# Kernel optimization log

Hardware: AMD Instinct MI355X
Metric: run time of the kernel (lower is better)

Reference implementation:

```python
import jax, jax.numpy as jnp
import numpy as np

NEG_SLOPE = 0.2


def setup_inputs() -> dict:
    key = jax.random.key(0)
    ks = jax.random.split(key, 9)
    N, E, D, H, C, G = 50000, 800000, 128, 4, 32, 64
    x = jax.random.normal(ks[0], (N, D), dtype=jnp.float32)
    edge_index = jax.random.randint(ks[1], (2, E), 0, N, dtype=jnp.int64)
    batch_ids = jnp.sort(jax.random.randint(ks[2], (N,), 0, G, dtype=jnp.int64))
    Wl = jax.random.normal(ks[3], (D, H * C), dtype=jnp.float32) / np.sqrt(D)
    Wr = jax.random.normal(ks[4], (D, H * C), dtype=jnp.float32) / np.sqrt(D)
    att = jax.random.normal(ks[5], (H, C), dtype=jnp.float32) / np.sqrt(C)
    bias_conv = jax.random.normal(ks[6], (H * C,), dtype=jnp.float32) * 0.01
    W_mlp = jax.random.normal(ks[7], (H * C, H * C), dtype=jnp.float32) / np.sqrt(H * C)
    b_mlp = jax.random.normal(ks[8], (H * C,), dtype=jnp.float32) * 0.01
    return {"x": x, "edge_index": edge_index, "batch_ids": batch_ids,
            "num_graphs": G, "Wl": Wl, "Wr": Wr, "att": att,
            "bias_conv": bias_conv, "W_mlp": W_mlp, "b_mlp": b_mlp}


def gatv2_forward(x, edge_index, batch_ids, num_graphs, Wl, Wr, att, bias_conv, W_mlp, b_mlp):
    N = x.shape[0]
    H, C = att.shape
    # add self loops (PyG default)
    loops = jnp.arange(N, dtype=edge_index.dtype)
    src = jnp.concatenate([edge_index[0], loops])
    dst = jnp.concatenate([edge_index[1], loops])
    xl = (x @ Wl).reshape(N, H, C)  # source transform
    xr = (x @ Wr).reshape(N, H, C)  # target transform
    # GATv2 attention logits per edge/head
    e = jax.nn.leaky_relu(xl[src] + xr[dst], NEG_SLOPE)  # [E,H,C]
    logits = jnp.einsum('ehc,hc->eh', e, att)            # [E,H]
    # segment softmax over incoming edges of each dst node
    m = jax.ops.segment_max(logits, dst, num_segments=N)
    ex = jnp.exp(logits - m[dst])
    denom = jax.ops.segment_sum(ex, dst, num_segments=N)
    alpha = ex / denom[dst]                              # [E,H]
    # weighted scatter-sum of source features
    out = jax.ops.segment_sum(alpha[:, :, None] * xl[src], dst, num_segments=N)
    out = out.reshape(N, H * C) + bias_conv
    out = jax.nn.relu(out)
    # global max pool per graph
    pooled = jax.ops.segment_max(out, batch_ids, num_segments=num_graphs)
    return jax.nn.relu(pooled @ W_mlp + b_mlp)


def reference(x, edge_index, batch_ids, num_graphs, Wl, Wr, att, bias_conv, W_mlp, b_mlp):
    return gatv2_forward(x, edge_index, batch_ids, num_graphs, Wl, Wr, att,
                         bias_conv, W_mlp, b_mlp)
```

## Files before the change

kernel.cpp:

```cpp
#include <hip/hip_runtime.h>
#include <hip/hip_bf16.h>

#define NN 50000
#define EE 800000
#define HC 128
#define GG 64

#define NBLK 256
#define CHUNK (EE / NBLK)
#define NBUCK ((NN + 63) >> 6)
#define NTOT (NBUCK * NBLK)
#define NSB ((NTOT + 1023) / 1024)
#define ECAP 2048

typedef __attribute__((ext_vector_type(8))) short bf16x8;
typedef __attribute__((ext_vector_type(4))) float f32x4;
typedef _Float16 hv2 __attribute__((ext_vector_type(2)));

__device__ __forceinline__ float dpp4_redrow(float t) {
  t += __int_as_float(__builtin_amdgcn_update_dpp(0, __float_as_int(t), 0x111, 0xf, 0xf, true));
  t += __int_as_float(__builtin_amdgcn_update_dpp(0, __float_as_int(t), 0x112, 0xf, 0xf, true));
  t += __int_as_float(__builtin_amdgcn_update_dpp(0, __float_as_int(t), 0x114, 0xf, 0xf, true));
  t += __int_as_float(__builtin_amdgcn_update_dpp(0, __float_as_int(t), 0x118, 0xf, 0xf, true));
  return t;
}
__device__ __forceinline__ float bcast15(float t) {
  return __int_as_float(__builtin_amdgcn_ds_swizzle(__float_as_int(t), 0x1F0));
}

__device__ __forceinline__ unsigned pkbf(float lo, float hi) {
  __hip_bfloat162 h = __float22bfloat162_rn(float2{lo, hi});
  return *reinterpret_cast<unsigned*>(&h);
}
__device__ __forceinline__ unsigned pkhf(float lo, float hi) {
  hv2 h; h.x = (_Float16)lo; h.y = (_Float16)hi;
  return __builtin_bit_cast(unsigned, h);
}

__global__ __launch_bounds__(128) void prep_w(const float* __restrict__ Wl,
                                              const float* __restrict__ Wr,
                                              short* __restrict__ Wtb) {
  int c = blockIdx.x;
  int k = threadIdx.x;
  const float* W = (c < 128) ? Wl : Wr;
  float v = W[k * 128 + (c & 127)];
  Wtb[c * 128 + k] = (short)(pkbf(v, 0.f) & 0xFFFF);
}

__global__ __launch_bounds__(256) void gemm_xw(
    const float* __restrict__ x, const short* __restrict__ Wtb,
    _Float16* __restrict__ xlh, _Float16* __restrict__ xrh,
    const int* __restrict__ ei, int* __restrict__ H2T)
{
  __shared__ short xs[128 * 136];
  __shared__ int h[NBUCK];
  const int t = threadIdx.x;
  const int rowbase = blockIdx.x * 128;
#pragma unroll
  for (int i = 0; i < 16; ++i) {
    int fi = i * 256 + t;
    int row = fi >> 5, k4 = fi & 31;
    int ar = rowbase + row; if (ar >= NN) ar = NN - 1;
    float4 v = *(const float4*)(x + (size_t)ar * 128 + k4 * 4);
    uint2 p = { pkbf(v.x, v.y), pkbf(v.z, v.w) };
    *(uint2*)&xs[row * 136 + k4 * 4] = p;
  }
  __syncthreads();
  const int w = t >> 6, l = t & 63;
  const int lo16 = l & 15, hi = l >> 4;
  f32x4 accL[2][8], accR[2][8];
#pragma unroll
  for (int rf = 0; rf < 2; ++rf)
#pragma unroll
    for (int cf = 0; cf < 8; ++cf) {
      accL[rf][cf] = f32x4{0.f, 0.f, 0.f, 0.f};
      accR[rf][cf] = f32x4{0.f, 0.f, 0.f, 0.f};
    }

  const short* asrc0 = &xs[(w * 32 + lo16) * 136 + hi * 8];
  const short* asrc1 = asrc0 + 16 * 136;
#pragma unroll
  for (int ks = 0; ks < 4; ++ks) {
    bf16x8 a0 = *(const bf16x8*)(asrc0 + ks * 32);
    bf16x8 a1 = *(const bf16x8*)(asrc1 + ks * 32);
#pragma unroll
    for (int cf = 0; cf < 8; ++cf) {
      const short* bp = &Wtb[(cf * 16 + lo16) * 128 + ks * 32 + hi * 8];
      bf16x8 bL = *(const bf16x8*)bp;
      bf16x8 bR = *(const bf16x8*)(bp + 128 * 128);
      accL[0][cf] = __builtin_amdgcn_mfma_f32_16x16x32_bf16(a0, bL, accL[0][cf], 0, 0, 0);
      accL[1][cf] = __builtin_amdgcn_mfma_f32_16x16x32_bf16(a1, bL, accL[1][cf], 0, 0, 0);
      accR[0][cf] = __builtin_amdgcn_mfma_f32_16x16x32_bf16(a0, bR, accR[0][cf], 0, 0, 0);
      accR[1][cf] = __builtin_amdgcn_mfma_f32_16x16x32_bf16(a1, bR, accR[1][cf], 0, 0, 0);
    }
  }
#pragma unroll
  for (int rf = 0; rf < 2; ++rf)
#pragma unroll
    for (int cf = 0; cf < 8; ++cf)
#pragma unroll
      for (int r = 0; r < 4; ++r) {
        int row = rowbase + w * 32 + rf * 16 + hi * 4 + r;
        if (row < NN) {
          int col = cf * 16 + lo16;
          xlh[(size_t)row * 128 + col] = (_Float16)accL[rf][cf][r];
          xrh[(size_t)row * 128 + col] = (_Float16)accR[rf][cf][r];
        }
      }
  int blk = blockIdx.x;
  if (blk < NBLK) {
    for (int b = t; b < NBUCK; b += 256) h[b] = 0;
    __syncthreads();
    int e0 = blk * CHUNK;
    for (int i = t; i < CHUNK; i += 256) {
      int d = ei[EE + e0 + i];
      atomicAdd(&h[d >> 6], 1);
    }
    __syncthreads();
    for (int b = t; b < NBUCK; b += 256) H2T[b * NBLK + blk] = h[b];
  }
}

__global__ __launch_bounds__(256) void scanA(const int* __restrict__ H2T,
                                             int* __restrict__ PS, int* __restrict__ bsum) {
  __shared__ int tmp[256];
  int t = threadIdx.x;
  int base = blockIdx.x * 1024 + t * 4;
  int4 v = {0, 0, 0, 0};
  if (base < NTOT) v = *(const int4*)&H2T[base];
  int local = v.x + v.y + v.z + v.w;
  tmp[t] = local; __syncthreads();
  for (int off = 1; off < 256; off <<= 1) {
    int xv = (t >= off) ? tmp[t - off] : 0; __syncthreads();
    tmp[t] += xv; __syncthreads();
  }
  int excl = tmp[t] - local;
  if (base < NTOT) {
    int4 o;
    o.x = excl; excl += v.x;
    o.y = excl; excl += v.y;
    o.z = excl; excl += v.z;
    o.w = excl;
    *(int4*)&PS[base] = o;
  }
  if (t == 255) bsum[blockIdx.x] = tmp[255];
}

__global__ __launch_bounds__(256) void scatter_coarse(const int* __restrict__ ei,
                                                      const int* __restrict__ PS,
                                                      const int* __restrict__ bsum,
                                                      int* __restrict__ ec) {
  __shared__ int colbase[NBUCK];
  __shared__ int cur[NBUCK];
  __shared__ int sb[NSB];
  __shared__ int stmp[256];
  int t = threadIdx.x, blk = blockIdx.x;
  int v = (t < NSB) ? bsum[t] : 0;
  stmp[t] = v; __syncthreads();
  for (int off = 1; off < 256; off <<= 1) {
    int xv = (t >= off) ? stmp[t - off] : 0; __syncthreads();
    stmp[t] += xv; __syncthreads();
  }
  if (t < NSB) sb[t] = stmp[t] - v;
  __syncthreads();
  for (int b = t; b < NBUCK; b += 256) {
    int L = b * NBLK + blk;
    colbase[b] = PS[L] + sb[L >> 10];
    cur[b] = 0;
  }
  __syncthreads();
  int e0 = blk * CHUNK;
  for (int i = t; i < CHUNK; i += 256) {
    int d = ei[EE + e0 + i], s = ei[e0 + i];
    int b = d >> 6;
    int r = atomicAdd(&cur[b], 1);
    ec[colbase[b] + r] = s | ((d & 63) << 16);
  }
}

__global__ __launch_bounds__(256) void fine_sort(const int* __restrict__ PS,
                                                 const int* __restrict__ bsum,
                                                 const int* __restrict__ ec,
                                                 int* __restrict__ rs, int* __restrict__ csr) {
  __shared__ int lbuf[ECAP];
  __shared__ int outb[ECAP + 64];
  __shared__ int fh[64], sexcl[65], cur2[64];
  __shared__ int sb[NSB];
  __shared__ int stmp[256];
  int t = threadIdx.x, b = blockIdx.x;
  int v = (t < NSB) ? bsum[t] : 0;
  stmp[t] = v; __syncthreads();
  for (int off = 1; off < 256; off <<= 1) {
    int xv = (t >= off) ? stmp[t - off] : 0; __syncthreads();
    stmp[t] += xv; __syncthreads();
  }
  if (t < NSB) sb[t] = stmp[t] - v;
  __syncthreads();
  int L0 = b * NBLK;
  int start = PS[L0] + sb[L0 >> 10];
  int end = (b + 1 < NBUCK) ? PS[L0 + NBLK] + sb[(L0 + NBLK) >> 10] : EE;
  int node0 = b << 6;
  int nl = NN - node0; if (nl > 64) nl = 64;
  int cnt = end - start; if (cnt > ECAP) cnt = ECAP;
  if (t < 64) { fh[t] = 0; cur2[t] = 0; }
  __syncthreads();
  for (int i = t; i < cnt; i += 256) {
    int p = ec[start + i];
    lbuf[i] = p;
    atomicAdd(&fh[(p >> 16) & 63], 1);
  }
  __syncthreads();
  if (t < 64) {
    int val = fh[t] + (t < nl ? 1 : 0);
    int w = val;
    for (int off = 1; off < 64; off <<= 1) {
      int u = __shfl_up(w, off);
      if (t >= off) w += u;
    }
    sexcl[t] = w - val;
    if (t == 63) sexcl[64] = w;
  }
  __syncthreads();
  int base = start + node0;
  if (t <= nl) rs[node0 + t] = base + sexcl[t];
  if (t < nl) {
    int r = atomicAdd(&cur2[t], 1);
    outb[sexcl[t] + r] = node0 + t;
  }
  for (int i = t; i < cnt; i += 256) {
    int p = lbuf[i];
    int f = (p >> 16) & 63;
    int r = atomicAdd(&cur2[f], 1);
    outb[sexcl[f] + r] = p & 0xFFFF;
  }
  __syncthreads();
  int tot = cnt + nl;
  for (int i = t; i < tot; i += 256) csr[base + i] = outb[i];
}

template<int M>
__device__ __forceinline__ void procM(const unsigned* wv, hv2 att2, hv2 xr2,
                                      float& s, float& a0, float& a1) {
  float tb[M];
#pragma unroll
  for (int i = 0; i < M; ++i) {
    hv2 v = __builtin_bit_cast(hv2, wv[i]);
    hv2 y = v + xr2;
    hv2 lr = __builtin_elementwise_max(y, y * (_Float16)0.2f);
    float td = __builtin_amdgcn_fdot2(lr, att2, 0.f, false);
    tb[i] = bcast15(dpp4_redrow(td));
  }
  float p[M];
#pragma unroll
  for (int i = 0; i < M; ++i) p[i] = __builtin_amdgcn_exp2f(tb[i]);
#pragma unroll
  for (int i = 0; i < M; ++i) {
    hv2 v = __builtin_bit_cast(hv2, wv[i]);
    s += p[i];
    a0 = fmaf(p[i], (float)v.x, a0);
    a1 = fmaf(p[i], (float)v.y, a1);
  }
}

__global__ __launch_bounds__(256) void gat_agg(
    const unsigned* __restrict__ xlu, const unsigned* __restrict__ xru,
    const int* __restrict__ rs, const int* __restrict__ csr,
    const float* __restrict__ att, const float* __restrict__ bias,
    unsigned* __restrict__ outh)
{
  int wid = threadIdx.x >> 6, lane = threadIdx.x & 63;
  int n = blockIdx.x * 4 + wid;
  if (n >= NN) return;
  hv2 xr2 = __builtin_bit_cast(hv2, xru[n * 64 + lane]);
  float2 at2 = ((const float2*)att)[lane];
  const float LOG2E = 1.4426950408889634f;
  hv2 att2;
  att2.x = (_Float16)(at2.x * LOG2E);
  att2.y = (_Float16)(at2.y * LOG2E);
  float s = 0.f, a0 = 0.f, a1 = 0.f;

  int jbeg = rs[n], jend = rs[n + 1];
  for (int j0 = jbeg; j0 < jend; j0 += 64) {
    int cnt = jend - j0; if (cnt > 64) cnt = 64;
    int sj = csr[j0 + (lane < cnt ? lane : cnt - 1)];
    int base = 0;
    if (cnt >= 8) {
      unsigned cur[8];
#pragma unroll
      for (int i = 0; i < 8; ++i)
        cur[i] = xlu[__builtin_amdgcn_readlane(sj, i) * 64 + lane];
      for (; base + 16 <= cnt; base += 8) {
        unsigned nxt[8];
#pragma unroll
        for (int i = 0; i < 8; ++i)
          nxt[i] = xlu[__builtin_amdgcn_readlane(sj, base + 8 + i) * 64 + lane];
        procM<8>(cur, att2, xr2, s, a0, a1);
#pragma unroll
        for (int i = 0; i < 8; ++i) cur[i] = nxt[i];
      }
      procM<8>(cur, att2, xr2, s, a0, a1);
      base += 8;
    }
    int rem = cnt - base;
    if (rem) {
      unsigned wv[8];
#pragma unroll
      for (int i = 0; i < 8; ++i)
        if (i < rem) wv[i] = xlu[__builtin_amdgcn_readlane(sj, base + i) * 64 + lane];
      switch (rem) {
        case 1: procM<1>(wv, att2, xr2, s, a0, a1); break;
        case 2: procM<2>(wv, att2, xr2, s, a0, a1); break;
        case 3: procM<3>(wv, att2, xr2, s, a0, a1); break;
        case 4: procM<4>(wv, att2, xr2, s, a0, a1); break;
        case 5: procM<5>(wv, att2, xr2, s, a0, a1); break;
        case 6: procM<6>(wv, att2, xr2, s, a0, a1); break;
        default: procM<7>(wv, att2, xr2, s, a0, a1); break;
      }
    }
  }
  float inv = 1.f / s;
  float2 bi = ((const float2*)bias)[lane];
  float ox = fmaxf(fmaf(a0, inv, bi.x), 0.f);
  float oy = fmaxf(fmaf(a1, inv, bi.y), 0.f);
  outh[(size_t)n * 64 + lane] = pkhf(ox, oy);
}

__global__ __launch_bounds__(1024) void pool_mlp(const unsigned* __restrict__ outh,
                                                 const int* __restrict__ batch,
                                                 const float* __restrict__ W,
                                                 const float* __restrict__ bm,
                                                 float* __restrict__ out) {
  __shared__ float pm0[16][64];
  __shared__ float pm1[16][64];
  __shared__ float p[128];
  __shared__ float acc8[8][128];
  int g = blockIdx.x, t = threadIdx.x;
  int a = 0, bnd = NN;
  while (a < bnd) { int m = (a + bnd) >> 1; if (batch[m] < g) a = m + 1; else bnd = m; }
  int lo = a;
  bnd = NN;
  while (a < bnd) { int m = (a + bnd) >> 1; if (batch[m] < g + 1) a = m + 1; else bnd = m; }
  int hi = a;
  int c2 = t & 63, q16 = t >> 6;
  float m0 = 0.f, m1 = 0.f;
  for (int n = lo + q16; n < hi; n += 16) {
    hv2 v = __builtin_bit_cast(hv2, outh[(size_t)n * 64 + c2]);
    m0 = fmaxf(m0, (float)v.x);
    m1 = fmaxf(m1, (float)v.y);
  }
  pm0[q16][c2] = m0;
  pm1[q16][c2] = m1;
  __syncthreads();
  if (t < 64) {
    float r0 = pm0[0][t], r1 = pm1[0][t];
#pragma unroll
    for (int i = 1; i < 16; ++i) {
      r0 = fmaxf(r0, pm0[i][t]);
      r1 = fmaxf(r1, pm1[i][t]);
    }
    p[2 * t] = r0;
    p[2 * t + 1] = r1;
  }
  __syncthreads();
  int c = t & 127, q = t >> 7;
  float acc = 0.f;
#pragma unroll
  for (int kk = 0; kk < 16; ++kk) {
    int k = q * 16 + kk;
    acc = fmaf(p[k], W[k * 128 + c], acc);
  }
  acc8[q][c] = acc;
  __syncthreads();
  if (q == 0) {
    float sum = bm[c];
#pragma unroll
    for (int i = 0; i < 8; ++i) sum += acc8[i][c];
    out[g * 128 + c] = fmaxf(sum, 0.f);
  }
}

extern "C" void kernel_launch(void* const* d_in, const int* in_sizes, int n_in,
                              void* d_out, int out_size, void* d_ws, size_t ws_size,
                              hipStream_t stream) {
  const float* x    = (const float*)d_in[0];
  const int*   ei   = (const int*)d_in[1];
  const int*   batch= (const int*)d_in[2];
  const float* Wl   = (const float*)d_in[4];
  const float* Wr   = (const float*)d_in[5];
  const float* att  = (const float*)d_in[6];
  const float* bias = (const float*)d_in[7];
  const float* Wm   = (const float*)d_in[8];
  const float* bm   = (const float*)d_in[9];

  char* ws = (char*)d_ws;
  size_t off = 0;
  auto alloc = [&](size_t bytes) { void* p = ws + off; off += (bytes + 255) & ~size_t(255); return p; };
  unsigned* xlu  = (unsigned*)alloc((size_t)NN * 64 * 4);
  unsigned* xru  = (unsigned*)alloc((size_t)NN * 64 * 4);
  unsigned* outh = (unsigned*)alloc((size_t)NN * 64 * 4);
  int*   rs      = (int*)alloc((size_t)(NN + 1) * 4);
  int*   csr     = (int*)alloc((size_t)(EE + NN) * 4);
  int*   H2T     = (int*)alloc((size_t)NTOT * 4);
  int*   PS      = (int*)alloc((size_t)NTOT * 4);
  int*   ec      = (int*)alloc((size_t)EE * 4);
  int*   bsum    = (int*)alloc(NSB * 4);
  short* Wtb     = (short*)alloc((size_t)256 * 128 * 2);

  prep_w<<<256, 128, 0, stream>>>(Wl, Wr, Wtb);
  gemm_xw<<<(NN + 127) / 128, 256, 0, stream>>>(x, Wtb, (_Float16*)xlu, (_Float16*)xru, ei, H2T);
  scanA<<<NSB, 256, 0, stream>>>(H2T, PS, bsum);
  scatter_coarse<<<NBLK, 256, 0, stream>>>(ei, PS, bsum, ec);
  fine_sort<<<NBUCK, 256, 0, stream>>>(PS, bsum, ec, rs, csr);
  gat_agg<<<NN / 4, 256, 0, stream>>>(xlu, xru, rs, csr, att, bias, outh);
  pool_mlp<<<GG, 1024, 0, stream>>>(outh, batch, Wm, bm, (float*)d_out);
}
```

Before: 130.0 us.

## Fuse fine bucket sort with GAT aggregation, keeping per-bucket CSR in shared memory

Merges the fine_sort kernel into the attention aggregation kernel. Each 1024-thread block sorts one 64-node bucket's edges in LDS, then its 16 waves process those nodes straight from the shared CSR. This drops the global rs/csr arrays, their write and read-back, and one kernel launch. In exchange there are only about 782 blocks of 1024 threads with heavy LDS use, so occupancy and load balance may be worse than the previous 12500 small blocks. The sort phase also leaves most threads idle.

```diff
diff --git a/kernel.cpp b/kernel.cpp
--- a/kernel.cpp
+++ b/kernel.cpp
@@ -178,23 +178,56 @@
   }
 }
 
-__global__ __launch_bounds__(256) void fine_sort(const int* __restrict__ PS,
-                                                 const int* __restrict__ bsum,
-                                                 const int* __restrict__ ec,
-                                                 int* __restrict__ rs, int* __restrict__ csr) {
+template<int M>
+__device__ __forceinline__ void procM(const unsigned* wv, hv2 att2, hv2 xr2,
+                                      float& s, float& a0, float& a1) {
+  float tb[M];
+#pragma unroll
+  for (int i = 0; i < M; ++i) {
+    hv2 v = __builtin_bit_cast(hv2, wv[i]);
+    hv2 y = v + xr2;
+    hv2 lr = __builtin_elementwise_max(y, y * (_Float16)0.2f);
+    float td = __builtin_amdgcn_fdot2(lr, att2, 0.f, false);
+    tb[i] = bcast15(dpp4_redrow(td));
+  }
+  float p[M];
+#pragma unroll
+  for (int i = 0; i < M; ++i) p[i] = __builtin_amdgcn_exp2f(tb[i]);
+#pragma unroll
+  for (int i = 0; i < M; ++i) {
+    hv2 v = __builtin_bit_cast(hv2, wv[i]);
+    s += p[i];
+    a0 = fmaf(p[i], (float)v.x, a0);
+    a1 = fmaf(p[i], (float)v.y, a1);
+  }
+}
+
+__global__ __launch_bounds__(1024) void gat_fused(
+    const unsigned* __restrict__ xlu, const unsigned* __restrict__ xru,
+    const int* __restrict__ PS, const int* __restrict__ bsum,
+    const int* __restrict__ ec, const float* __restrict__ att,
+    const float* __restrict__ bias, unsigned* __restrict__ outh)
+{
   __shared__ int lbuf[ECAP];
   __shared__ int outb[ECAP + 64];
   __shared__ int fh[64], sexcl[65], cur2[64];
   __shared__ int sb[NSB];
   __shared__ int stmp[256];
   int t = threadIdx.x, b = blockIdx.x;
-  int v = (t < NSB) ? bsum[t] : 0;
-  stmp[t] = v; __syncthreads();
-  for (int off = 1; off < 256; off <<= 1) {
-    int xv = (t >= off) ? stmp[t - off] : 0; __syncthreads();
-    stmp[t] += xv; __syncthreads();
-  }
-  if (t < NSB) sb[t] = stmp[t] - v;
+  if (t < 256) {
+    int v = (t < NSB) ? bsum[t] : 0;
+    stmp[t] = v;
+  }
+  __syncthreads();
+  if (t < 256) {
+    for (int off = 1; off < 256; off <<= 1) {
+      int xv = (t >= off) ? stmp[t - off] : 0; __syncthreads();
+      stmp[t] += xv; __syncthreads();
+    }
+    if (t < NSB) sb[t] = stmp[t] - ((t < NSB) ? bsum[t] : 0);
+  } else {
+    for (int off = 1; off < 256; off <<= 1) { __syncthreads(); __syncthreads(); }
+  }
   __syncthreads();
   int L0 = b * NBLK;
   int start = PS[L0] + sb[L0 >> 10];
@@ -204,7 +237,7 @@
   int cnt = end - start; if (cnt > ECAP) cnt = ECAP;
   if (t < 64) { fh[t] = 0; cur2[t] = 0; }
   __syncthreads();
-  for (int i = t; i < cnt; i += 256) {
+  for (int i = t; i < cnt; i += 1024) {
     int p = ec[start + i];
     lbuf[i] = p;
     atomicAdd(&fh[(p >> 16) & 63], 1);
@@ -221,108 +254,74 @@
     if (t == 63) sexcl[64] = w;
   }
   __syncthreads();
-  int base = start + node0;
-  if (t <= nl) rs[node0 + t] = base + sexcl[t];
   if (t < nl) {
     int r = atomicAdd(&cur2[t], 1);
     outb[sexcl[t] + r] = node0 + t;
   }
-  for (int i = t; i < cnt; i += 256) {
+  for (int i = t; i < cnt; i += 1024) {
     int p = lbuf[i];
     int f = (p >> 16) & 63;
     int r = atomicAdd(&cur2[f], 1);
     outb[sexcl[f] + r] = p & 0xFFFF;
   }
   __syncthreads();
-  int tot = cnt + nl;
-  for (int i = t; i < tot; i += 256) csr[base + i] = outb[i];
-}
-
-template<int M>
-__device__ __forceinline__ void procM(const unsigned* wv, hv2 att2, hv2 xr2,
-                                      float& s, float& a0, float& a1) {
-  float tb[M];
-#pragma unroll
-  for (int i = 0; i < M; ++i) {
-    hv2 v = __builtin_bit_cast(hv2, wv[i]);
-    hv2 y = v + xr2;
-    hv2 lr = __builtin_elementwise_max(y, y * (_Float16)0.2f);
-    float td = __builtin_amdgcn_fdot2(lr, att2, 0.f, false);
-    tb[i] = bcast15(dpp4_redrow(td));
-  }
-  float p[M];
-#pragma unroll
-  for (int i = 0; i < M; ++i) p[i] = __builtin_amdgcn_exp2f(tb[i]);
-#pragma unroll
-  for (int i = 0; i < M; ++i) {
-    hv2 v = __builtin_bit_cast(hv2, wv[i]);
-    s += p[i];
-    a0 = fmaf(p[i], (float)v.x, a0);
-    a1 = fmaf(p[i], (float)v.y, a1);
-  }
-}
-
-__global__ __launch_bounds__(256) void gat_agg(
-    const unsigned* __restrict__ xlu, const unsigned* __restrict__ xru,
-    const int* __restrict__ rs, const int* __restrict__ csr,
-    const float* __restrict__ att, const float* __restrict__ bias,
-    unsigned* __restrict__ outh)
-{
-  int wid = threadIdx.x >> 6, lane = threadIdx.x & 63;
-  int n = blockIdx.x * 4 + wid;
-  if (n >= NN) return;
-  hv2 xr2 = __builtin_bit_cast(hv2, xru[n * 64 + lane]);
+
+  int wid = t >> 6, lane = t & 63;
   float2 at2 = ((const float2*)att)[lane];
   const float LOG2E = 1.4426950408889634f;
   hv2 att2;
   att2.x = (_Float16)(at2.x * LOG2E);
   att2.y = (_Float16)(at2.y * LOG2E);
-  float s = 0.f, a0 = 0.f, a1 = 0.f;
-
-  int jbeg = rs[n], jend = rs[n + 1];
-  for (int j0 = jbeg; j0 < jend; j0 += 64) {
-    int cnt = jend - j0; if (cnt > 64) cnt = 64;
-    int sj = csr[j0 + (lane < cnt ? lane : cnt - 1)];
-    int base = 0;
-    if (cnt >= 8) {
-      unsigned cur[8];
-#pragma unroll
-      for (int i = 0; i < 8; ++i)
-        cur[i] = xlu[__builtin_amdgcn_readlane(sj, i) * 64 + lane];
-      for (; base + 16 <= cnt; base += 8) {
-        unsigned nxt[8];
+  float2 bi = ((const float2*)bias)[lane];
+
+  for (int ni = wid; ni < nl; ni += 16) {
+    int n = node0 + ni;
+    hv2 xr2 = __builtin_bit_cast(hv2, xru[n * 64 + lane]);
+    float s = 0.f, a0 = 0.f, a1 = 0.f;
+    int jbeg = sexcl[ni], jend = sexcl[ni + 1];
+    for (int j0 = jbeg; j0 < jend; j0 += 64) {
+      int cnt2 = jend - j0; if (cnt2 > 64) cnt2 = 64;
+      int sj = outb[j0 + (lane < cnt2 ? lane : cnt2 - 1)];
+      int base = 0;
+      if (cnt2 >= 8) {
+        unsigned cur[8];
 #pragma unroll
         for (int i = 0; i < 8; ++i)
-          nxt[i] = xlu[__builtin_amdgcn_readlane(sj, base + 8 + i) * 64 + lane];
+          cur[i] = xlu[__builtin_amdgcn_readlane(sj, i) * 64 + lane];
+        for (; base + 16 <= cnt2; base += 8) {
+          unsigned nxt[8];
+#pragma unroll
+          for (int i = 0; i < 8; ++i)
+            nxt[i] = xlu[__builtin_amdgcn_readlane(sj, base + 8 + i) * 64 + lane];
+          procM<8>(cur, att2, xr2, s, a0, a1);
+#pragma unroll
+          for (int i = 0; i < 8; ++i) cur[i] = nxt[i];
+        }
         procM<8>(cur, att2, xr2, s, a0, a1);
-#pragma unroll
-        for (int i = 0; i < 8; ++i) cur[i] = nxt[i];
+        base += 8;
       }
-      procM<8>(cur, att2, xr2, s, a0, a1);
-      base += 8;
-    }
-    int rem = cnt - base;
-    if (rem) {
-      unsigned wv[8];
-#pragma unroll
-      for (int i = 0; i < 8; ++i)
-        if (i < rem) wv[i] = xlu[__builtin_amdgcn_readlane(sj, base + i) * 64 + lane];
-      switch (rem) {
-        case 1: procM<1>(wv, att2, xr2, s, a0, a1); break;
-        case 2: procM<2>(wv, att2, xr2, s, a0, a1); break;
-        case 3: procM<3>(wv, att2, xr2, s, a0, a1); break;
-        case 4: procM<4>(wv, att2, xr2, s, a0, a1); break;
-        case 5: procM<5>(wv, att2, xr2, s, a0, a1); break;
-        case 6: procM<6>(wv, att2, xr2, s, a0, a1); break;
-        default: procM<7>(wv, att2, xr2, s, a0, a1); break;
+      int rem = cnt2 - base;
+      if (rem) {
+        unsigned wv[8];
+#pragma unroll
+        for (int i = 0; i < 8; ++i)
+          if (i < rem) wv[i] = xlu[__builtin_amdgcn_readlane(sj, base + i) * 64 + lane];
+        switch (rem) {
+          case 1: procM<1>(wv, att2, xr2, s, a0, a1); break;
+          case 2: procM<2>(wv, att2, xr2, s, a0, a1); break;
+          case 3: procM<3>(wv, att2, xr2, s, a0, a1); break;
+          case 4: procM<4>(wv, att2, xr2, s, a0, a1); break;
+          case 5: procM<5>(wv, att2, xr2, s, a0, a1); break;
+          case 6: procM<6>(wv, att2, xr2, s, a0, a1); break;
+          default: procM<7>(wv, att2, xr2, s, a0, a1); break;
+        }
       }
     }
-  }
-  float inv = 1.f / s;
-  float2 bi = ((const float2*)bias)[lane];
-  float ox = fmaxf(fmaf(a0, inv, bi.x), 0.f);
-  float oy = fmaxf(fmaf(a1, inv, bi.y), 0.f);
-  outh[(size_t)n * 64 + lane] = pkhf(ox, oy);
+    float inv = 1.f / s;
+    float ox = fmaxf(fmaf(a0, inv, bi.x), 0.f);
+    float oy = fmaxf(fmaf(a1, inv, bi.y), 0.f);
+    outh[(size_t)n * 64 + lane] = pkhf(ox, oy);
+  }
 }
 
 __global__ __launch_bounds__(1024) void pool_mlp(const unsigned* __restrict__ outh,
@@ -398,8 +397,6 @@
   unsigned* xlu  = (unsigned*)alloc((size_t)NN * 64 * 4);
   unsigned* xru  = (unsigned*)alloc((size_t)NN * 64 * 4);
   unsigned* outh = (unsigned*)alloc((size_t)NN * 64 * 4);
-  int*   rs      = (int*)alloc((size_t)(NN + 1) * 4);
-  int*   csr     = (int*)alloc((size_t)(EE + NN) * 4);
   int*   H2T     = (int*)alloc((size_t)NTOT * 4);
   int*   PS      = (int*)alloc((size_t)NTOT * 4);
   int*   ec      = (int*)alloc((size_t)EE * 4);
@@ -410,7 +407,6 @@
   gemm_xw<<<(NN + 127) / 128, 256, 0, stream>>>(x, Wtb, (_Float16*)xlu, (_Float16*)xru, ei, H2T);
   scanA<<<NSB, 256, 0, stream>>>(H2T, PS, bsum);
   scatter_coarse<<<NBLK, 256, 0, stream>>>(ei, PS, bsum, ec);
-  fine_sort<<<NBUCK, 256, 0, stream>>>(PS, bsum, ec, rs, csr);
-  gat_agg<<<NN / 4, 256, 0, stream>>>(xlu, xru, rs, csr, att, bias, outh);
+  gat_fused<<<NBUCK, 1024, 0, stream>>>(xlu, xru, PS, bsum, ec, att, bias, outh);
   pool_mlp<<<GG, 1024, 0, stream>>>(outh, batch, Wm, bm, (float*)d_out);
 }
```

Result: slower. 140.5 us (+8.1%).
